# Performance work log

Hardware: AMD Instinct MI355X
Metric: run time of the kernel (lower is better)

## Reference

```python
import jax, jax.numpy as jnp
import numpy as np

B, LX, LY, D = 64, 1024, 1024, 300

def setup_inputs() -> dict:
    key = jax.random.key(0)
    kx, ky, kw, kb = jax.random.split(key, 4)
    x = jax.random.normal(kx, (B, LX, D), dtype=jnp.float32)
    y = jax.random.normal(ky, (B, LY, D), dtype=jnp.float32)
    # True = padded position (masked out); mask last quarter so rows are never fully masked
    y_mask = jnp.arange(LY)[None, :] >= (3 * LY // 4)
    y_mask = jnp.broadcast_to(y_mask, (B, LY))
    # shared Linear(embed_dim, embed_dim) params (PyTorch default uniform init)
    bound = 1.0 / np.sqrt(D)
    W = jax.random.uniform(kw, (D, D), minval=-bound, maxval=bound, dtype=jnp.float32)
    b = jax.random.uniform(kb, (D,), minval=-bound, maxval=bound, dtype=jnp.float32)
    return {"x": x, "y": y, "y_mask": y_mask, "W": W, "b": b}

def reference(x, y, y_mask, W, b):
    # shared projection: Linear + ReLU applied to both x and y
    x_proj = jax.nn.relu(jnp.einsum("bsd,ed->bse", x, W) + b)   # (B, Lx, D)
    y_proj = jax.nn.relu(jnp.einsum("btd,ed->bte", y, W) + b)   # (B, Ly, D)
    scores = jnp.einsum("bse,bte->bst", x_proj, y_proj)          # (B, Lx, Ly)
    neg_inf = jnp.finfo(scores.dtype).min
    scores = jnp.where(y_mask[:, None, :], neg_inf, scores)
    weights = jax.nn.softmax(scores, axis=2)
    contexts = jnp.einsum("bst,btd->bsd", weights, y)            # (B, Lx, D)
    return contexts
```

## Files before the change

kernel.cpp:

```cpp
#include <hip/hip_runtime.h>
#include <cmath>

#define B_   64
#define LX_  1024
#define LY_  1024
#define D_   300
#define DP   320
#define DV   304
#define BM   64
#define KV   32
#define NT   (LY_ / KV)

using f32x4  = __attribute__((ext_vector_type(4))) float;
using bf16x8 = __attribute__((ext_vector_type(8))) __bf16;
using u32x4  = __attribute__((ext_vector_type(4))) unsigned int;
using u32x2  = __attribute__((ext_vector_type(2))) unsigned int;

static __device__ __forceinline__ unsigned short f2b(float f){
    unsigned u = __builtin_bit_cast(unsigned, f);
    u += 0x7FFFu + ((u >> 16) & 1u);
    return (unsigned short)(u >> 16);
}

static __device__ __forceinline__ unsigned pk_bf16(float lo, float hi){
    unsigned r;
    asm volatile("v_cvt_pk_bf16_f32 %0, %1, %2" : "=v"(r) : "v"(lo), "v"(hi));
    return r;
}

static __device__ __forceinline__ bf16x8 ld_bf8(const unsigned short* p){
    u32x4 u = *(const u32x4*)p;
    return __builtin_bit_cast(bf16x8, u);
}

static __device__ __forceinline__ f32x4 mfma16(bf16x8 a, bf16x8 b, f32x4 c){
    return __builtin_amdgcn_mfma_f32_16x16x32_bf16(a, b, c, 0, 0, 0);
}

__global__ __launch_bounds__(256) void k_pre(const float* __restrict__ Y,
        const int* __restrict__ mask, const float* __restrict__ W,
        unsigned short* __restrict__ yT, unsigned short* __restrict__ Wb){
    const int bid = blockIdx.x;
    const int tid = threadIdx.x;

    if (bid >= 5120){
        const int i = (bid - 5120) * 256 + tid;
        if (i < DP * DP){
            const int e = i / DP, d = i % DP;
            float v = (e < D_ && d < D_) ? W[e * D_ + d] : 0.f;
            Wb[i] = f2b(v);
        }
        return;
    }

    __shared__ float tile[64][65];
    const int b  = bid / 80;
    const int tt = (bid % 80) / 5;
    const int dt = bid % 5;
    const int t0 = tt * 64, d0 = dt * 64;
    const int dl = tid & 63, qq = tid >> 6;

    const int mv = mask[b * LY_ + t0 + dl];
    if (__all(mv != 0)) return;

    #pragma unroll
    for (int r = 0; r < 16; ++r){
        const int tl = qq * 16 + r;
        const int d = d0 + dl;
        float v = (d < D_) ? Y[((long)b * LY_ + t0 + tl) * D_ + d] : 0.f;
        tile[tl][dl] = v;
    }
    __syncthreads();
    #pragma unroll
    for (int r = 0; r < 16; ++r){
        const int drow = d0 + qq * 16 + r;
        if (drow < DV){
            float v = (drow < D_) ? tile[dl][qq * 16 + r] : 0.f;
            yT[((long)b * DV + drow) * LY_ + t0 + dl] = f2b(v);
        }
    }
}

__global__ __launch_bounds__(256) void k_proj(const float* __restrict__ X,
        const float* __restrict__ Y, const float* __restrict__ bias,
        const int* __restrict__ mask, const unsigned short* __restrict__ Wb,
        unsigned short* __restrict__ Px, unsigned short* __restrict__ Py){
    const int tid = threadIdx.x;
    const int w = tid >> 6, l = tid & 63;
    const int lr = l & 15, lg = l >> 4;
    const long m0 = (long)blockIdx.x * 128;
    const bool isX = (m0 < (long)B_ * LX_);
    const float* S = isX ? X : Y;
    unsigned short* Dst = isX ? Px : Py;
    const long base = isX ? m0 : m0 - (long)B_ * LX_;

    if (!isX){
        const int bb = (int)(base >> 10);
        const int trow = ((int)base & 1023) + 32 * w + (l & 31);
        const int mv = mask[bb * LY_ + trow];
        if (__all(mv != 0)) return;
    }

    u32x4 a[2][10];
    #pragma unroll
    for (int ms = 0; ms < 2; ++ms){
        const float* rp = S + (base + 32 * w + 16 * ms + lr) * D_;
        #pragma unroll
        for (int ks = 0; ks < 10; ++ks){
            const int k0 = ks * 32 + lg * 8;
            f32x4 v0 = {0,0,0,0}, v1 = {0,0,0,0};
            if (k0 + 4 <= D_) v0 = *(const f32x4*)(rp + k0);
            if (k0 + 8 <= D_) v1 = *(const f32x4*)(rp + k0 + 4);
            u32x4 u;
            u[0] = pk_bf16(v0[0], v0[1]);
            u[1] = pk_bf16(v0[2], v0[3]);
            u[2] = pk_bf16(v1[0], v1[1]);
            u[3] = pk_bf16(v1[2], v1[3]);
            a[ms][ks] = u;
        }
    }

    #pragma unroll 2
    for (int es = 0; es < 20; ++es){
        f32x4 acc0 = {0,0,0,0}, acc1 = {0,0,0,0};
        const unsigned short* wp = Wb + (es * 16 + lr) * DP + lg * 8;
        #pragma unroll
        for (int ks = 0; ks < 10; ++ks){
            bf16x8 bf = ld_bf8(wp + ks * 32);
            acc0 = mfma16(bf, __builtin_bit_cast(bf16x8, a[0][ks]), acc0);
            acc1 = mfma16(bf, __builtin_bit_cast(bf16x8, a[1][ks]), acc1);
        }
        const int e0 = es * 16 + lg * 4;
        f32x4 bv = {0,0,0,0};
        if (e0 + 4 <= D_) bv = *(const f32x4*)(bias + e0);
        else {
            #pragma unroll
            for (int r = 0; r < 4; ++r) bv[r] = (e0 + r < D_) ? bias[e0 + r] : 0.f;
        }
        float s0[4], s1[4];
        #pragma unroll
        for (int r = 0; r < 4; ++r){
            float t0v = acc0[r] + bv[r]; s0[r] = t0v > 0.f ? t0v : 0.f;
            float t1v = acc1[r] + bv[r]; s1[r] = t1v > 0.f ? t1v : 0.f;
        }
        const u32x2 o0 = { pk_bf16(s0[0], s0[1]), pk_bf16(s0[2], s0[3]) };
        const u32x2 o1 = { pk_bf16(s1[0], s1[1]), pk_bf16(s1[2], s1[3]) };
        *(u32x2*)(Dst + (base + 32 * w + lr) * DP + e0)      = o0;
        *(u32x2*)(Dst + (base + 32 * w + 16 + lr) * DP + e0) = o1;
    }
}

__global__ __launch_bounds__(256, 2) void k_attn(const int* __restrict__ mask,
        const unsigned short* __restrict__ Px, const unsigned short* __restrict__ Py,
        const unsigned short* __restrict__ yT, float* __restrict__ out){
    __shared__ unsigned short Yp_lds[KV][320];
    __shared__ unsigned short yT_lds[DV][32];
    __shared__ unsigned short P_lds[BM][40];

    const int tid = threadIdx.x;
    const int w = tid >> 6, l = tid & 63;
    const int lr = l & 15, lg = l >> 4;
    const int sw3 = lr & 7;
    const int s2  = (lr >> 1) & 3;

    const int bid = blockIdx.x;
    const int xcd = bid & 7;
    const int g = bid >> 3;
    const int b = xcd + 8 * (g >> 4);
    const int s0 = (g & 15) * BM;

    u32x4 q[10];
    {
        const unsigned short* qp = Px + ((long)b * LX_ + s0 + 16 * w + lr) * DP + lg * 8;
        #pragma unroll
        for (int ks = 0; ks < 10; ++ks) q[ks] = *(const u32x4*)(qp + ks * 32);
    }

    const unsigned short* srcYp[5];
    unsigned short*       dstYp[5];
    #pragma unroll
    for (int j = 0; j < 5; ++j){
        const int id = tid + 256 * j;
        const int row = id / 40, c = id % 40;
        srcYp[j] = Py + ((long)b * LY_ + row) * DP + c * 8;
        dstYp[j] = &Yp_lds[row][(c ^ (row & 7)) * 8];
    }
    const unsigned short* srcYT[5];
    unsigned short*       dstYT[5];
    #pragma unroll
    for (int j = 0; j < 5; ++j){
        const int id = tid + 256 * j;
        const int row = (id >> 2) < DV ? (id >> 2) : (DV - 1);
        const int c = id & 3;
        srcYT[j] = yT + ((long)b * DV + row) * LY_ + c * 8;
        dstYT[j] = &yT_lds[row][(c ^ ((row >> 1) & 3)) * 8];
    }
    const bool v4 = (tid < 192);

    const int* mrow = mask + (long)b * LY_;

    u32x4 pA[5], pT[5];
    #pragma unroll
    for (int j = 0; j < 5; ++j) pA[j] = *(const u32x4*)srcYp[j];
    #pragma unroll
    for (int j = 0; j < 4; ++j) pT[j] = *(const u32x4*)srcYT[j];
    if (v4) pT[4] = *(const u32x4*)srcYT[4];
    int4 m0v = *(const int4*)(mrow + lg * 4);
    int4 m1v = *(const int4*)(mrow + 16 + lg * 4);
    #pragma unroll
    for (int j = 0; j < 5; ++j) *(u32x4*)dstYp[j] = pA[j];
    #pragma unroll
    for (int j = 0; j < 4; ++j) *(u32x4*)dstYT[j] = pT[j];
    if (v4) *(u32x4*)dstYT[4] = pT[4];
    __syncthreads();

    f32x4 acc[19];
    #pragma unroll
    for (int n = 0; n < 19; ++n) acc[n] = f32x4{0,0,0,0};
    float m_r = -INFINITY;
    float l_r = 0.f;

    for (int it = 0; it < NT; ++it){
        const bool notlast = (it < NT - 1);

        int4 mn0, mn1;
        if (notlast){
            #pragma unroll
            for (int j = 0; j < 5; ++j){ srcYp[j] += KV * DP; pA[j] = *(const u32x4*)srcYp[j]; }
            #pragma unroll
            for (int j = 0; j < 4; ++j){ srcYT[j] += KV;      pT[j] = *(const u32x4*)srcYT[j]; }
            srcYT[4] += KV;
            if (v4) pT[4] = *(const u32x4*)srcYT[4];
            mn0 = *(const int4*)(mrow + (it + 1) * KV + lg * 4);
            mn1 = *(const int4*)(mrow + (it + 1) * KV + 16 + lg * 4);
        }

        const int allm = (m0v.x && m0v.y && m0v.z && m0v.w &&
                          m1v.x && m1v.y && m1v.z && m1v.w) ? 1 : 0;
        if (!__all(allm)){
            f32x4 sv0 = {0,0,0,0}, sv1 = {0,0,0,0};
            #pragma unroll
            for (int ks = 0; ks < 10; ++ks){
                const int cc = (((ks << 2) | lg) ^ sw3) << 3;
                bf16x8 qf = __builtin_bit_cast(bf16x8, q[ks]);
                bf16x8 a0 = ld_bf8(&Yp_lds[lr][cc]);
                bf16x8 a1 = ld_bf8(&Yp_lds[16 + lr][cc]);
                sv0 = mfma16(a0, qf, sv0);
                sv1 = mfma16(a1, qf, sv1);
            }

            float v0[4], v1[4];
            v0[0] = sv0[0] + (m0v.x ? -3.0e38f : 0.f);
            v0[1] = sv0[1] + (m0v.y ? -3.0e38f : 0.f);
            v0[2] = sv0[2] + (m0v.z ? -3.0e38f : 0.f);
            v0[3] = sv0[3] + (m0v.w ? -3.0e38f : 0.f);
            v1[0] = sv1[0] + (m1v.x ? -3.0e38f : 0.f);
            v1[1] = sv1[1] + (m1v.y ? -3.0e38f : 0.f);
            v1[2] = sv1[2] + (m1v.z ? -3.0e38f : 0.f);
            v1[3] = sv1[3] + (m1v.w ? -3.0e38f : 0.f);

            float mx = fmaxf(fmaxf(fmaxf(v0[0], v0[1]), fmaxf(v0[2], v0[3])),
                             fmaxf(fmaxf(v1[0], v1[1]), fmaxf(v1[2], v1[3])));
            mx = fmaxf(mx, __shfl_xor(mx, 16));
            mx = fmaxf(mx, __shfl_xor(mx, 32));
            const float nm = fmaxf(m_r, mx);

            float p0[4], p1[4];
            float ps = 0.f;
            #pragma unroll
            for (int r = 0; r < 4; ++r){
                p0[r] = __expf(v0[r] - nm);
                p1[r] = __expf(v1[r] - nm);
                ps += p0[r] + p1[r];
            }
            ps += __shfl_xor(ps, 16);
            ps += __shfl_xor(ps, 32);
            const float sc = __expf(m_r - nm);
            l_r = l_r * sc + ps;
            m_r = nm;

            float scr[4];
            #pragma unroll
            for (int r = 0; r < 4; ++r) scr[r] = __shfl(sc, lg * 4 + r);
            #pragma unroll
            for (int n = 0; n < 19; ++n){
                #pragma unroll
                for (int r = 0; r < 4; ++r) acc[n][r] *= scr[r];
            }

            const unsigned c00 = pk_bf16(p0[0], p0[1]);
            const unsigned c01 = pk_bf16(p0[2], p0[3]);
            const unsigned c10 = pk_bf16(p1[0], p1[1]);
            const unsigned c11 = pk_bf16(p1[2], p1[3]);
            *(u32x2*)&P_lds[16 * w + lr][4 * lg]      = u32x2{c00, c01};
            *(u32x2*)&P_lds[16 * w + lr][16 + 4 * lg] = u32x2{c10, c11};

            bf16x8 pf = ld_bf8(&P_lds[16 * w + lr][lg * 8]);
            const int vcc = (lg ^ s2) << 3;
            #pragma unroll
            for (int n = 0; n < 19; ++n){
                bf16x8 vf = ld_bf8(&yT_lds[n * 16 + lr][vcc]);
                acc[n] = mfma16(pf, vf, acc[n]);
            }
        }

        __syncthreads();
        if (notlast){
            #pragma unroll
            for (int j = 0; j < 5; ++j) *(u32x4*)dstYp[j] = pA[j];
            #pragma unroll
            for (int j = 0; j < 4; ++j) *(u32x4*)dstYT[j] = pT[j];
            if (v4) *(u32x4*)dstYT[4] = pT[4];
            m0v = mn0; m1v = mn1;
        }
        __syncthreads();
    }

    const float il = 1.f / l_r;
    float invr[4];
    #pragma unroll
    for (int r = 0; r < 4; ++r) invr[r] = __shfl(il, lg * 4 + r);

    #pragma unroll
    for (int n = 0; n < 19; ++n){
        const int d = n * 16 + lr;
        if (d < D_){
            #pragma unroll
            for (int r = 0; r < 4; ++r){
                out[((long)b * LX_ + s0 + 16 * w + lg * 4 + r) * D_ + d] = acc[n][r] * invr[r];
            }
        }
    }
}

extern "C" void kernel_launch(void* const* d_in, const int* in_sizes, int n_in,
                              void* d_out, int out_size, void* d_ws, size_t ws_size,
                              hipStream_t stream){
    const float* x = (const float*)d_in[0];
    const float* y = (const float*)d_in[1];
    const int* ymask = (const int*)d_in[2];
    const float* W = (const float*)d_in[3];
    const float* bias = (const float*)d_in[4];
    float* out = (float*)d_out;

    unsigned short* Wb  = (unsigned short*)d_ws;
    unsigned short* Px  = (unsigned short*)((char*)d_ws + (1 << 18));
    unsigned short* Py  = (unsigned short*)((char*)d_ws + (1 << 18) + 41943040LL);
    unsigned short* yTw = (unsigned short*)((char*)d_ws + (1 << 18) + 83886080LL);

    hipLaunchKernelGGL(k_pre,  dim3(5520), dim3(256), 0, stream, y, ymask, W, yTw, Wb);
    hipLaunchKernelGGL(k_proj, dim3(1024), dim3(256), 0, stream, x, y, bias, ymask, Wb, Px, Py);
    hipLaunchKernelGGL(k_attn, dim3(1024), dim3(256), 0, stream, ymask, Px, Py, yTw, out);
}
```

Measured before the change: 301.3 us.

## Stage projection weights through double-buffered swizzled LDS in k_proj

The projection kernel previously had every wave read its weight fragments straight from global memory. It now cooperatively loads 32-row slices of W into a double-buffered, XOR-swizzled LDS buffer, prefetching the next slice into registers while the MFMAs run on the current one. The masked-row skip check is also changed from a per-wave vote to a block-wide shared flag, so the early return happens before any __syncthreads. The change adds about 40KB of LDS per block and a barrier per slice, which can reduce occupancy.

```diff
diff --git a/kernel.cpp b/kernel.cpp
--- a/kernel.cpp
+++ b/kernel.cpp
@@ -85,21 +85,30 @@
         const float* __restrict__ Y, const float* __restrict__ bias,
         const int* __restrict__ mask, const unsigned short* __restrict__ Wb,
         unsigned short* __restrict__ Px, unsigned short* __restrict__ Py){
+    __shared__ unsigned short Wl[2][32][320];
+    __shared__ int s_skip;
+
     const int tid = threadIdx.x;
     const int w = tid >> 6, l = tid & 63;
     const int lr = l & 15, lg = l >> 4;
+    const int sw3 = lr & 7;
     const long m0 = (long)blockIdx.x * 128;
     const bool isX = (m0 < (long)B_ * LX_);
     const float* S = isX ? X : Y;
     unsigned short* Dst = isX ? Px : Py;
     const long base = isX ? m0 : m0 - (long)B_ * LX_;
 
+    int unmask = 1;
     if (!isX){
         const int bb = (int)(base >> 10);
-        const int trow = ((int)base & 1023) + 32 * w + (l & 31);
-        const int mv = mask[bb * LY_ + trow];
-        if (__all(mv != 0)) return;
-    }
+        const int trow = ((int)base & 1023) + (tid & 127);
+        unmask = (mask[bb * LY_ + trow] == 0) ? 1 : 0;
+    }
+    if (tid == 0) s_skip = 1;
+    __syncthreads();
+    if (unmask) s_skip = 0;
+    __syncthreads();
+    if (s_skip) return;
 
     u32x4 a[2][10];
     #pragma unroll
@@ -120,33 +129,72 @@
         }
     }
 
-    #pragma unroll 2
-    for (int es = 0; es < 20; ++es){
-        f32x4 acc0 = {0,0,0,0}, acc1 = {0,0,0,0};
-        const unsigned short* wp = Wb + (es * 16 + lr) * DP + lg * 8;
+    const unsigned short* srcW[5];
+    int offW[5];
+    #pragma unroll
+    for (int j = 0; j < 5; ++j){
+        const int id = tid + 256 * j;
+        const int row = id / 40, c = id % 40;
+        srcW[j] = Wb + row * DP + c * 8;
+        offW[j] = row * 320 + (c ^ (row & 7)) * 8;
+    }
+    unsigned short* const WlBase = &Wl[0][0][0];
+
+    u32x4 pW[5];
+    #pragma unroll
+    for (int j = 0; j < 5; ++j) pW[j] = *(const u32x4*)srcW[j];
+    #pragma unroll
+    for (int j = 0; j < 5; ++j) *(u32x4*)(WlBase + offW[j]) = pW[j];
+    __syncthreads();
+
+    int cur = 0;
+    #pragma unroll 1
+    for (int sl = 0; sl < 10; ++sl){
+        const bool notlast = (sl < 9);
+        if (notlast){
+            #pragma unroll
+            for (int j = 0; j < 5; ++j){ srcW[j] += 32 * DP; pW[j] = *(const u32x4*)srcW[j]; }
+        }
+
+        const unsigned short* Wc = WlBase + cur * 10240;
         #pragma unroll
-        for (int ks = 0; ks < 10; ++ks){
-            bf16x8 bf = ld_bf8(wp + ks * 32);
-            acc0 = mfma16(bf, __builtin_bit_cast(bf16x8, a[0][ks]), acc0);
-            acc1 = mfma16(bf, __builtin_bit_cast(bf16x8, a[1][ks]), acc1);
-        }
-        const int e0 = es * 16 + lg * 4;
-        f32x4 bv = {0,0,0,0};
-        if (e0 + 4 <= D_) bv = *(const f32x4*)(bias + e0);
-        else {
-            #pragma unroll
-            for (int r = 0; r < 4; ++r) bv[r] = (e0 + r < D_) ? bias[e0 + r] : 0.f;
-        }
-        float s0[4], s1[4];
-        #pragma unroll
-        for (int r = 0; r < 4; ++r){
-            float t0v = acc0[r] + bv[r]; s0[r] = t0v > 0.f ? t0v : 0.f;
-            float t1v = acc1[r] + bv[r]; s1[r] = t1v > 0.f ? t1v : 0.f;
-        }
-        const u32x2 o0 = { pk_bf16(s0[0], s0[1]), pk_bf16(s0[2], s0[3]) };
-        const u32x2 o1 = { pk_bf16(s1[0], s1[1]), pk_bf16(s1[2], s1[3]) };
-        *(u32x2*)(Dst + (base + 32 * w + lr) * DP + e0)      = o0;
-        *(u32x2*)(Dst + (base + 32 * w + 16 + lr) * DP + e0) = o1;
+        for (int es2 = 0; es2 < 2; ++es2){
+            const int es = 2 * sl + es2;
+            f32x4 acc0 = {0,0,0,0}, acc1 = {0,0,0,0};
+            const unsigned short* wrow = Wc + (es2 * 16 + lr) * 320;
+            #pragma unroll
+            for (int ks = 0; ks < 10; ++ks){
+                const int cc = (((ks << 2) | lg) ^ sw3) << 3;
+                bf16x8 bf = ld_bf8(wrow + cc);
+                acc0 = mfma16(bf, __builtin_bit_cast(bf16x8, a[0][ks]), acc0);
+                acc1 = mfma16(bf, __builtin_bit_cast(bf16x8, a[1][ks]), acc1);
+            }
+            const int e0 = es * 16 + lg * 4;
+            f32x4 bv = {0,0,0,0};
+            if (e0 + 4 <= D_) bv = *(const f32x4*)(bias + e0);
+            else {
+                #pragma unroll
+                for (int r = 0; r < 4; ++r) bv[r] = (e0 + r < D_) ? bias[e0 + r] : 0.f;
+            }
+            float s0[4], s1[4];
+            #pragma unroll
+            for (int r = 0; r < 4; ++r){
+                float t0v = acc0[r] + bv[r]; s0[r] = t0v > 0.f ? t0v : 0.f;
+                float t1v = acc1[r] + bv[r]; s1[r] = t1v > 0.f ? t1v : 0.f;
+            }
+            const u32x2 o0 = { pk_bf16(s0[0], s0[1]), pk_bf16(s0[2], s0[3]) };
+            const u32x2 o1 = { pk_bf16(s1[0], s1[1]), pk_bf16(s1[2], s1[3]) };
+            *(u32x2*)(Dst + (base + 32 * w + lr) * DP + e0)      = o0;
+            *(u32x2*)(Dst + (base + 32 * w + 16 + lr) * DP + e0) = o1;
+        }
+
+        if (notlast){
+            unsigned short* Wn = WlBase + (cur ^ 1) * 10240;
+            #pragma unroll
+            for (int j = 0; j < 5; ++j) *(u32x4*)(Wn + offW[j]) = pW[j];
+        }
+        __syncthreads();
+        cur ^= 1;
     }
 }
 
```

New measurement: 248.7 us. 1.21x faster.
